# Kernel optimization log

Hardware: AMD Instinct MI355X
Metric: run time of the kernel (lower is better)

The kernel has to match this reference:

```python
import jax, jax.numpy as jnp
import numpy as np

C = 256

def setup_inputs() -> dict:
    key = jax.random.key(0)
    k1, k2, k3, k4, k5 = jax.random.split(key, 5)
    x = jax.random.normal(k1, (4, C, 64, 64), dtype=jnp.float32)
    # conv1x1 weights stored as (out, in) matrices
    w_qkv = jax.random.normal(k2, (3 * C, C), dtype=jnp.float32) * (1.0 / np.sqrt(C))
    b_qkv = jax.random.normal(k3, (3 * C,), dtype=jnp.float32) * 0.01
    w_out = jax.random.normal(k4, (C, C), dtype=jnp.float32) * (1.0 / np.sqrt(C))
    b_out = jax.random.normal(k5, (C,), dtype=jnp.float32) * 0.01
    return {"x": x, "w_qkv": w_qkv, "b_qkv": b_qkv, "w_out": w_out, "b_out": b_out}

def reference(x, w_qkv, b_qkv, w_out, b_out):
    b, c, h, w = x.shape
    # norm = Identity. conv1x1 == channel matmul
    qkv = jnp.einsum('bchw,oc->bohw', x, w_qkv) + b_qkv[None, :, None, None]
    q, k, v = jnp.split(qkv, 3, axis=1)  # each (b, c, h, w)
    q = q.reshape(b, c, h * w).transpose(0, 2, 1)  # (b, hw, c)
    k = k.reshape(b, c, h * w)                      # (b, c, hw)
    v = v.reshape(b, c, h * w).transpose(0, 2, 1)  # (b, hw, c)
    scores = jnp.einsum('bnc,bcm->bnm', q, k) * (c ** -0.5)  # (b, hw, hw)
    attn = jax.nn.softmax(scores, axis=-1)
    out = jnp.einsum('bnm,bmc->bnc', attn, v)  # (b, hw, c)
    out = out.transpose(0, 2, 1).reshape(b, c, h, w)
    out = jnp.einsum('bchw,oc->bohw', out, w_out) + b_out[None, :, None, None]
    return out + x
```

## Files before the change

kernel.cpp:

```cpp
#include <hip/hip_runtime.h>
#include <hip/hip_bf16.h>
#include <hip/hip_fp16.h>
#include <math.h>

typedef short s16x8 __attribute__((ext_vector_type(8)));
typedef float f32x4 __attribute__((ext_vector_type(4)));
typedef float f32x16 __attribute__((ext_vector_type(16)));
typedef unsigned short u16x4 __attribute__((ext_vector_type(4)));

#define CCH 256
#define SEQ 4096
#define NB 4
#define KVB 32

static __device__ __forceinline__ unsigned short f2bf(float f) {
  union { float f; unsigned int u; } v; v.f = f;
  unsigned int u = v.u;
  unsigned int r = u + 0x7FFFu + ((u >> 16) & 1u);
  return (unsigned short)(r >> 16);
}

static __device__ __forceinline__ void gl16(const void* g, void* l) {
  __builtin_amdgcn_global_load_lds(
      (const __attribute__((address_space(1))) void*)g,
      (__attribute__((address_space(3))) void*)l, 16, 0, 0);
}

__global__ __launch_bounds__(256) void cvt_wall(
    const float* __restrict__ wqkv, const float* __restrict__ wout,
    unsigned short* __restrict__ wqkb, unsigned short* __restrict__ wob)
{
  int bid = blockIdx.x;
  const float* src;
  unsigned short* dst;
  int i;
  if (bid < 192) { src = wqkv; dst = wqkb; i = bid * 256 + threadIdx.x; }
  else           { src = wout; dst = wob;  i = (bid - 192) * 256 + threadIdx.x; }
  float4 v = ((const float4*)src)[i];
  u16x4 r;
  r.x = f2bf(v.x); r.y = f2bf(v.y); r.z = f2bf(v.z); r.w = f2bf(v.w);
  ((u16x4*)dst)[i] = r;
}

__global__ __launch_bounds__(256) void cvt_x(const float* __restrict__ x,
                                             unsigned short* __restrict__ xb) {
  __shared__ unsigned short T[64][72];
  int b = blockIdx.z, ct = blockIdx.y, st = blockIdx.x;
  int c0 = ct * 64, s0 = st * 64;
  int tid = threadIdx.x;
  #pragma unroll
  for (int i = 0; i < 4; i++) {
    int idx = tid + i * 256;
    int cr = idx >> 4, c4 = idx & 15;
    float4 v = *(const float4*)&x[((size_t)b * CCH + c0 + cr) * SEQ + s0 + c4 * 4];
    #pragma unroll
    for (int j = 0; j < 4; j++) {
      int s = c4 * 4 + j;
      int colp = cr ^ ((((s) >> 1) & 7) << 3);
      float fv = (j == 0) ? v.x : (j == 1) ? v.y : (j == 2) ? v.z : v.w;
      T[s][colp] = f2bf(fv);
    }
  }
  __syncthreads();
  #pragma unroll
  for (int i = 0; i < 2; i++) {
    int idx = tid + i * 256;
    int sr = idx >> 3, ch = idx & 7;
    int chp = ch ^ ((sr >> 1) & 7);
    s16x8 v = *(const s16x8*)&T[sr][chp * 8];
    *(s16x8*)&xb[((size_t)b * SEQ + s0 + sr) * CCH + c0 + ch * 8] = v;
  }
}

__global__ __launch_bounds__(256) void qk_proj(
    const unsigned short* __restrict__ xb, const unsigned short* __restrict__ wqkb,
    const float* __restrict__ bias,
    unsigned short* __restrict__ qb, unsigned short* __restrict__ kb)
{
  int b = blockIdx.y, st = blockIdx.x;
  int tid = threadIdx.x, w = tid >> 6, l = tid & 63, l15 = l & 15, lg = l >> 4;
  int row0 = st * 32 + (w & 1) * 16;
  int osel = w >> 1;

  const unsigned short* xp = xb + ((size_t)b * SEQ + row0 + l15) * CCH + lg * 8;
  s16x8 af[8];
  #pragma unroll
  for (int t = 0; t < 8; t++) af[t] = *(const s16x8*)(xp + t * 32);

  unsigned short* dst = osel ? kb : qb;
  #pragma unroll
  for (int ot = 0; ot < 16; ot++) {
    int orow = osel * 256 + ot * 16;
    f32x4 acc = (f32x4){0.f, 0.f, 0.f, 0.f};
    #pragma unroll
    for (int t = 0; t < 8; t++) {
      s16x8 wf = *(const s16x8*)&wqkb[(size_t)(orow + l15) * CCH + t * 32 + lg * 8];
      acc = __builtin_amdgcn_mfma_f32_16x16x32_bf16(af[t], wf, acc, 0, 0, 0);
    }
    float bi = bias[orow + l15];
    int ch = ot * 16 + l15;
    #pragma unroll
    for (int r = 0; r < 4; r++) {
      int srow = row0 + lg * 4 + r;
      dst[((size_t)b * SEQ + srow) * CCH + ch] = f2bf(acc[r] + bi);
    }
  }
}

__global__ __launch_bounds__(256) void v_proj(
    const unsigned short* __restrict__ xb, const unsigned short* __restrict__ wqkb,
    const float* __restrict__ bias, unsigned short* __restrict__ vb)
{
  int b = blockIdx.y, st = blockIdx.x;
  int tid = threadIdx.x, w = tid >> 6, l = tid & 63, l15 = l & 15, lg = l >> 4;
  int sbase = st * 32, obase = w * 64;

  f32x4 acc[4][2];
  #pragma unroll
  for (int i = 0; i < 4; i++)
    #pragma unroll
    for (int j = 0; j < 2; j++) acc[i][j] = (f32x4){0.f, 0.f, 0.f, 0.f};

  const unsigned short* xrow = xb + ((size_t)b * SEQ + sbase) * CCH;
  #pragma unroll
  for (int kt = 0; kt < 8; kt++) {
    s16x8 afr[4], bfr[2];
    #pragma unroll
    for (int ot = 0; ot < 4; ot++)
      afr[ot] = *(const s16x8*)&wqkb[(size_t)(512 + obase + ot * 16 + l15) * CCH + kt * 32 + lg * 8];
    #pragma unroll
    for (int sj = 0; sj < 2; sj++)
      bfr[sj] = *(const s16x8*)&xrow[(size_t)(sj * 16 + l15) * CCH + kt * 32 + lg * 8];
    #pragma unroll
    for (int ot = 0; ot < 4; ot++)
      #pragma unroll
      for (int sj = 0; sj < 2; sj++)
        acc[ot][sj] = __builtin_amdgcn_mfma_f32_16x16x32_bf16(afr[ot], bfr[sj], acc[ot][sj], 0, 0, 0);
  }

  #pragma unroll
  for (int ot = 0; ot < 4; ot++) {
    #pragma unroll
    for (int r = 0; r < 4; r++) {
      int o = obase + ot * 16 + lg * 4 + r;
      float bi = bias[512 + o];
      #pragma unroll
      for (int sj = 0; sj < 2; sj++) {
        int s = sbase + sj * 16 + l15;
        vb[((size_t)b * CCH + o) * SEQ + s] = f2bf(acc[ot][sj][r] + bi);
      }
    }
  }
}

template<int NSPLIT_>
__global__ __launch_bounds__(512, 2) void attn_kernel(
    const unsigned short* __restrict__ qb,
    const unsigned short* __restrict__ kb,
    const unsigned short* __restrict__ vb,
    __half* __restrict__ pacc, float* __restrict__ llp)
{
  constexpr int KVLEN_ = SEQ / NSPLIT_;
  constexpr int NT_ = KVLEN_ / KVB;
  __shared__ __align__(16) unsigned short Ks[2][KVB * CCH];
  __shared__ __align__(16) unsigned short Vs[2][CCH * KVB];
  __shared__ __align__(16) unsigned short plds[8][32][40];

  int b = blockIdx.z, kvh = blockIdx.y, qt = blockIdx.x;
  int tid = threadIdx.x, w = tid >> 6, l = tid & 63;
  int l31 = l & 31, lh = l >> 5;

  int qrow0 = qt * 256 + w * 32;
  const unsigned short* qptr = qb + ((size_t)b * SEQ + qrow0 + l31) * CCH + lh * 8;
  s16x8 qf[16];
  #pragma unroll
  for (int t = 0; t < 16; t++) qf[t] = *(const s16x8*)(qptr + t * 16);

  f32x16 oacc[8];
  #pragma unroll
  for (int i = 0; i < 8; i++)
    #pragma unroll
    for (int j = 0; j < 16; j++) oacc[i][j] = 0.f;
  float ll = 0.f;

  int koff0 = (tid >> 5) * CCH + (((tid & 31) ^ ((tid >> 5) & 7)) * 8);
  int voff0 = (tid >> 2) * SEQ + (((tid & 3) ^ ((tid >> 3) & 3)) * 8);
  const unsigned short* kbb = kb + (size_t)b * SEQ * CCH + (size_t)kvh * KVLEN_ * CCH;
  const unsigned short* vbb = vb + (size_t)b * CCH * SEQ + kvh * KVLEN_;

  auto stage = [&](int bf_, int kv) {
    #pragma unroll
    for (int i = 0; i < 2; i++)
      gl16(kbb + (size_t)kv * KVB * CCH + koff0 + i * 16 * CCH, &Ks[bf_][(i * 512 + tid) * 8]);
    #pragma unroll
    for (int i = 0; i < 2; i++)
      gl16(vbb + kv * KVB + voff0 + (size_t)i * 128 * SEQ, &Vs[bf_][(i * 512 + tid) * 8]);
  };

  stage(0, 0);
  __syncthreads();

  int buf = 0;
  int s7 = l31 & 7, sl = (l31 >> 1) & 3;
  for (int kv = 0; kv < NT_; kv++) {
    if (kv + 1 < NT_) stage(buf ^ 1, kv + 1);

    f32x16 sacc;
    #pragma unroll
    for (int i = 0; i < 16; i++) sacc[i] = 0.f;
    __builtin_amdgcn_s_setprio(1);
    #pragma unroll
    for (int st = 0; st < 16; st++) {
      s16x8 kf = *(const s16x8*)&Ks[buf][l31 * CCH + (((st * 2 + lh) ^ s7) * 8)];
      sacc = __builtin_amdgcn_mfma_f32_32x32x16_bf16(kf, qf[st], sacc, 0, 0, 0);
    }
    __builtin_amdgcn_s_setprio(0);

    #pragma unroll
    for (int rg = 0; rg < 4; rg++) {
      u16x4 pk;
      #pragma unroll
      for (int j = 0; j < 4; j++) {
        float p = exp2f(fmaf(sacc[rg * 4 + j], 0.09016844f, -11.5415602f));
        ll += p;
        ((unsigned short*)&pk)[j] = f2bf(p);
      }
      *(u16x4*)&plds[w][l31][rg * 8 + lh * 4] = pk;
    }

    s16x8 pa0 = *(const s16x8*)&plds[w][l31][lh * 8];
    s16x8 pa1 = *(const s16x8*)&plds[w][l31][16 + lh * 8];
    __builtin_amdgcn_s_setprio(1);
    #pragma unroll
    for (int dt = 0; dt < 8; dt++) {
      int chb = (dt * 32 + l31) * KVB;
      s16x8 vf0 = *(const s16x8*)&Vs[buf][chb + ((lh ^ sl) * 8)];
      oacc[dt] = __builtin_amdgcn_mfma_f32_32x32x16_bf16(pa0, vf0, oacc[dt], 0, 0, 0);
      s16x8 vf1 = *(const s16x8*)&Vs[buf][chb + (((2 + lh) ^ sl) * 8)];
      oacc[dt] = __builtin_amdgcn_mfma_f32_32x32x16_bf16(pa1, vf1, oacc[dt], 0, 0, 0);
    }
    __builtin_amdgcn_s_setprio(0);

    __syncthreads();
    buf ^= 1;
  }

  ll += __shfl_xor(ll, 32);
  size_t pbase = (size_t)(b * NSPLIT_ + kvh) * SEQ;
  if (lh == 0) llp[pbase + qrow0 + l31] = ll;
  __half* pb_ = pacc + (pbase + qrow0) * CCH + l31;
  #pragma unroll
  for (int rg = 0; rg < 4; rg++)
    #pragma unroll
    for (int j = 0; j < 4; j++) {
      int qr = j + 8 * rg + 4 * lh;
      #pragma unroll
      for (int dt = 0; dt < 8; dt++)
        pb_[(size_t)qr * CCH + dt * 32] = __float2half(oacc[dt][rg * 4 + j]);
    }
}

template<int NSPLIT_>
__global__ __launch_bounds__(256) void combine(
    const __half* __restrict__ pacc, const float* __restrict__ llp,
    unsigned short* __restrict__ aob)
{
  int idx = blockIdx.x * 256 + threadIdx.x;
  int c4 = idx & 63;
  int srow = idx >> 6;
  int b = srow >> 12, s = srow & 4095;
  float den = 0.f;
  float acc[4] = {0.f, 0.f, 0.f, 0.f};
  #pragma unroll
  for (int k = 0; k < NSPLIT_; k++) {
    size_t pb = (size_t)(b * NSPLIT_ + k) * SEQ + s;
    den += llp[pb];
    const __half* p = pacc + pb * CCH + c4 * 4;
    #pragma unroll
    for (int j = 0; j < 4; j++) acc[j] += __half2float(p[j]);
  }
  float inv = 1.f / den;
  u16x4 r;
  #pragma unroll
  for (int j = 0; j < 4; j++) ((unsigned short*)&r)[j] = f2bf(acc[j] * inv);
  *(u16x4*)&aob[((size_t)b * SEQ + s) * CCH + c4 * 4] = r;
}

__global__ __launch_bounds__(256) void out_proj(
    const unsigned short* __restrict__ aob, const unsigned short* __restrict__ wb,
    const float* __restrict__ bias, const float* __restrict__ x,
    float* __restrict__ out)
{
  int b = blockIdx.y, st = blockIdx.x;
  int tid = threadIdx.x, w = tid >> 6, l = tid & 63, l15 = l & 15, lg = l >> 4;
  int sbase = st * 32, obase = w * 64;

  f32x4 acc[4][2];
  #pragma unroll
  for (int i = 0; i < 4; i++)
    #pragma unroll
    for (int j = 0; j < 2; j++) acc[i][j] = (f32x4){0.f, 0.f, 0.f, 0.f};

  const unsigned short* aorow = aob + ((size_t)b * SEQ + sbase) * CCH;
  #pragma unroll
  for (int kt = 0; kt < 8; kt++) {
    s16x8 af[4], bfr[2];
    #pragma unroll
    for (int ot = 0; ot < 4; ot++)
      af[ot] = *(const s16x8*)&wb[(obase + ot * 16 + l15) * CCH + kt * 32 + lg * 8];
    #pragma unroll
    for (int sj = 0; sj < 2; sj++)
      bfr[sj] = *(const s16x8*)&aorow[(size_t)(sj * 16 + l15) * CCH + kt * 32 + lg * 8];
    #pragma unroll
    for (int ot = 0; ot < 4; ot++)
      #pragma unroll
      for (int sj = 0; sj < 2; sj++)
        acc[ot][sj] = __builtin_amdgcn_mfma_f32_16x16x32_bf16(af[ot], bfr[sj], acc[ot][sj], 0, 0, 0);
  }

  #pragma unroll
  for (int ot = 0; ot < 4; ot++) {
    #pragma unroll
    for (int r = 0; r < 4; r++) {
      int o = obase + ot * 16 + lg * 4 + r;
      float bi = bias[o];
      #pragma unroll
      for (int sj = 0; sj < 2; sj++) {
        int s = sbase + sj * 16 + l15;
        size_t idx = ((size_t)b * CCH + o) * SEQ + s;
        out[idx] = acc[ot][sj][r] + bi + x[idx];
      }
    }
  }
}

extern "C" void kernel_launch(void* const* d_in, const int* in_sizes, int n_in,
                              void* d_out, int out_size, void* d_ws, size_t ws_size,
                              hipStream_t stream) {
  const float* x     = (const float*)d_in[0];
  const float* w_qkv = (const float*)d_in[1];
  const float* b_qkv = (const float*)d_in[2];
  const float* w_out = (const float*)d_in[3];
  const float* b_out = (const float*)d_in[4];
  float* out = (float*)d_out;

  char* ws = (char*)d_ws;
  unsigned short* xbp  = (unsigned short*)(ws);
  unsigned short* qbp  = (unsigned short*)(ws + ((size_t)8 << 20));
  unsigned short* kbp  = (unsigned short*)(ws + ((size_t)16 << 20));
  unsigned short* vbp  = (unsigned short*)(ws + ((size_t)24 << 20));
  unsigned short* aob  = (unsigned short*)(ws + ((size_t)32 << 20));
  unsigned short* wqkb = (unsigned short*)(ws + ((size_t)40 << 20));
  unsigned short* wob  = (unsigned short*)(ws + ((size_t)40 << 20) + (512u << 10));
  float*          llp  = (float*)(ws + ((size_t)41 << 20));
  __half*         pacc = (__half*)(ws + ((size_t)42 << 20));

  cvt_wall<<<dim3(256), 256, 0, stream>>>(w_qkv, w_out, wqkb, wob);
  cvt_x<<<dim3(64, 4, NB), 256, 0, stream>>>(x, xbp);
  qk_proj<<<dim3(128, NB), 256, 0, stream>>>(xbp, wqkb, b_qkv, qbp, kbp);
  v_proj<<<dim3(128, NB), 256, 0, stream>>>(xbp, wqkb, b_qkv, vbp);

  bool split4 = ws_size >= ((size_t)76 << 20);
  if (split4) {
    attn_kernel<4><<<dim3(16, 4, NB), 512, 0, stream>>>(qbp, kbp, vbp, pacc, llp);
    combine<4><<<dim3(4096), 256, 0, stream>>>(pacc, llp, aob);
  } else {
    attn_kernel<2><<<dim3(16, 2, NB), 512, 0, stream>>>(qbp, kbp, vbp, pacc, llp);
    combine<2><<<dim3(4096), 256, 0, stream>>>(pacc, llp, aob);
  }
  out_proj<<<dim3(128, NB), 256, 0, stream>>>(aob, wob, b_out, x, out);
}
```

Before: 168.8 us.

## Double KV tile to 64 and keep P in registers via permlane swap

Raises the KV block from 32 to 64, so each iteration processes two 32-column halves and the number of barriers and staging rounds is halved. The LDS round-trip used to reshape softmax probabilities into the MFMA A-operand layout is replaced by packed bf16 conversion plus v_permlane32_swap in registers, and exp2f becomes the raw hardware exp2. The cost is doubled K/V shared memory (128 KB per block), which may conflict with the 2-blocks-per-CU launch bound and reduce occupancy.

```diff
diff --git a/kernel.cpp b/kernel.cpp
--- a/kernel.cpp
+++ b/kernel.cpp
@@ -7,11 +7,12 @@
 typedef float f32x4 __attribute__((ext_vector_type(4)));
 typedef float f32x16 __attribute__((ext_vector_type(16)));
 typedef unsigned short u16x4 __attribute__((ext_vector_type(4)));
+typedef unsigned int u32x4 __attribute__((ext_vector_type(4)));
 
 #define CCH 256
 #define SEQ 4096
 #define NB 4
-#define KVB 32
+#define KVB 64
 
 static __device__ __forceinline__ unsigned short f2bf(float f) {
   union { float f; unsigned int u; } v; v.f = f;
@@ -24,6 +25,12 @@
   __builtin_amdgcn_global_load_lds(
       (const __attribute__((address_space(1))) void*)g,
       (__attribute__((address_space(3))) void*)l, 16, 0, 0);
+}
+
+static __device__ __forceinline__ unsigned int cvt_pk_bf16(float lo, float hi) {
+  unsigned int w;
+  asm("v_cvt_pk_bf16_f32 %0, %1, %2" : "=v"(w) : "v"(lo), "v"(hi));
+  return w;
 }
 
 __global__ __launch_bounds__(256) void cvt_wall(
@@ -164,11 +171,11 @@
   constexpr int NT_ = KVLEN_ / KVB;
   __shared__ __align__(16) unsigned short Ks[2][KVB * CCH];
   __shared__ __align__(16) unsigned short Vs[2][CCH * KVB];
-  __shared__ __align__(16) unsigned short plds[8][32][40];
 
   int b = blockIdx.z, kvh = blockIdx.y, qt = blockIdx.x;
   int tid = threadIdx.x, w = tid >> 6, l = tid & 63;
   int l31 = l & 31, lh = l >> 5;
+  int s7 = l31 & 7;
 
   int qrow0 = qt * 256 + w * 32;
   const unsigned short* qptr = qb + ((size_t)b * SEQ + qrow0 + l31) * CCH + lh * 8;
@@ -184,62 +191,67 @@
   float ll = 0.f;
 
   int koff0 = (tid >> 5) * CCH + (((tid & 31) ^ ((tid >> 5) & 7)) * 8);
-  int voff0 = (tid >> 2) * SEQ + (((tid & 3) ^ ((tid >> 3) & 3)) * 8);
+  int voff0 = (tid >> 3) * SEQ + (((tid & 7) ^ ((tid >> 3) & 7)) * 8);
   const unsigned short* kbb = kb + (size_t)b * SEQ * CCH + (size_t)kvh * KVLEN_ * CCH;
   const unsigned short* vbb = vb + (size_t)b * CCH * SEQ + kvh * KVLEN_;
 
   auto stage = [&](int bf_, int kv) {
     #pragma unroll
-    for (int i = 0; i < 2; i++)
+    for (int i = 0; i < 4; i++)
       gl16(kbb + (size_t)kv * KVB * CCH + koff0 + i * 16 * CCH, &Ks[bf_][(i * 512 + tid) * 8]);
     #pragma unroll
-    for (int i = 0; i < 2; i++)
-      gl16(vbb + kv * KVB + voff0 + (size_t)i * 128 * SEQ, &Vs[bf_][(i * 512 + tid) * 8]);
+    for (int i = 0; i < 4; i++)
+      gl16(vbb + kv * KVB + voff0 + (size_t)i * 64 * SEQ, &Vs[bf_][(i * 512 + tid) * 8]);
   };
 
   stage(0, 0);
   __syncthreads();
 
   int buf = 0;
-  int s7 = l31 & 7, sl = (l31 >> 1) & 3;
   for (int kv = 0; kv < NT_; kv++) {
     if (kv + 1 < NT_) stage(buf ^ 1, kv + 1);
 
-    f32x16 sacc;
-    #pragma unroll
-    for (int i = 0; i < 16; i++) sacc[i] = 0.f;
-    __builtin_amdgcn_s_setprio(1);
-    #pragma unroll
-    for (int st = 0; st < 16; st++) {
-      s16x8 kf = *(const s16x8*)&Ks[buf][l31 * CCH + (((st * 2 + lh) ^ s7) * 8)];
-      sacc = __builtin_amdgcn_mfma_f32_32x32x16_bf16(kf, qf[st], sacc, 0, 0, 0);
-    }
-    __builtin_amdgcn_s_setprio(0);
-
-    #pragma unroll
-    for (int rg = 0; rg < 4; rg++) {
-      u16x4 pk;
-      #pragma unroll
-      for (int j = 0; j < 4; j++) {
-        float p = exp2f(fmaf(sacc[rg * 4 + j], 0.09016844f, -11.5415602f));
-        ll += p;
-        ((unsigned short*)&pk)[j] = f2bf(p);
-      }
-      *(u16x4*)&plds[w][l31][rg * 8 + lh * 4] = pk;
-    }
-
-    s16x8 pa0 = *(const s16x8*)&plds[w][l31][lh * 8];
-    s16x8 pa1 = *(const s16x8*)&plds[w][l31][16 + lh * 8];
-    __builtin_amdgcn_s_setprio(1);
-    #pragma unroll
-    for (int dt = 0; dt < 8; dt++) {
-      int chb = (dt * 32 + l31) * KVB;
-      s16x8 vf0 = *(const s16x8*)&Vs[buf][chb + ((lh ^ sl) * 8)];
-      oacc[dt] = __builtin_amdgcn_mfma_f32_32x32x16_bf16(pa0, vf0, oacc[dt], 0, 0, 0);
-      s16x8 vf1 = *(const s16x8*)&Vs[buf][chb + (((2 + lh) ^ sl) * 8)];
-      oacc[dt] = __builtin_amdgcn_mfma_f32_32x32x16_bf16(pa1, vf1, oacc[dt], 0, 0, 0);
-    }
-    __builtin_amdgcn_s_setprio(0);
+    #pragma unroll
+    for (int h = 0; h < 2; h++) {
+      f32x16 sacc;
+      #pragma unroll
+      for (int i = 0; i < 16; i++) sacc[i] = 0.f;
+      __builtin_amdgcn_s_setprio(1);
+      #pragma unroll
+      for (int st = 0; st < 16; st++) {
+        s16x8 kf = *(const s16x8*)&Ks[buf][(h * 32 + l31) * CCH + (((st * 2 + lh) ^ s7) * 8)];
+        sacc = __builtin_amdgcn_mfma_f32_32x32x16_bf16(kf, qf[st], sacc, 0, 0, 0);
+      }
+      __builtin_amdgcn_s_setprio(0);
+
+      unsigned int pw[8];
+      #pragma unroll
+      for (int r = 0; r < 8; r++) {
+        float p0 = __builtin_amdgcn_exp2f(fmaf(sacc[2 * r],     0.09016844f, -11.5415602f));
+        float p1 = __builtin_amdgcn_exp2f(fmaf(sacc[2 * r + 1], 0.09016844f, -11.5415602f));
+        ll += p0 + p1;
+        pw[r] = cvt_pk_bf16(p0, p1);
+      }
+      asm volatile("v_permlane32_swap_b32 %0, %1" : "+v"(pw[0]), "+v"(pw[2]));
+      asm volatile("v_permlane32_swap_b32 %0, %1" : "+v"(pw[1]), "+v"(pw[3]));
+      asm volatile("v_permlane32_swap_b32 %0, %1" : "+v"(pw[4]), "+v"(pw[6]));
+      asm volatile("v_permlane32_swap_b32 %0, %1" : "+v"(pw[5]), "+v"(pw[7]));
+      u32x4 pa0u = {pw[0], pw[1], pw[2], pw[3]};
+      u32x4 pa1u = {pw[4], pw[5], pw[6], pw[7]};
+      s16x8 pa0 = *(s16x8*)&pa0u;
+      s16x8 pa1 = *(s16x8*)&pa1u;
+
+      __builtin_amdgcn_s_setprio(1);
+      #pragma unroll
+      for (int dt = 0; dt < 8; dt++) {
+        int base = (dt * 32 + l31) * KVB;
+        s16x8 vf0 = *(const s16x8*)&Vs[buf][base + (((h * 4 + lh) ^ s7) * 8)];
+        oacc[dt] = __builtin_amdgcn_mfma_f32_32x32x16_bf16(pa0, vf0, oacc[dt], 0, 0, 0);
+        s16x8 vf1 = *(const s16x8*)&Vs[buf][base + (((h * 4 + 2 + lh) ^ s7) * 8)];
+        oacc[dt] = __builtin_amdgcn_mfma_f32_32x32x16_bf16(pa1, vf1, oacc[dt], 0, 0, 0);
+      }
+      __builtin_amdgcn_s_setprio(0);
+    }
 
     __syncthreads();
     buf ^= 1;
```

New measurement: 163.0 us. 1.04x faster.
